# Kernel tuning notes

Measured on AMD Instinct MI355X. Metric: run time of the kernel, lower is better.

Reference implementation:

```python
import jax, jax.numpy as jnp
import numpy as np

# LSNNParameters defaults (norse)
TAU_SYN_INV = 200.0     # 1/tau_syn
TAU_MEM_INV = 100.0     # 1/tau_mem
TAU_ADAPT_INV = 1.0 / 800.0  # 1/tau_adapt
V_LEAK = 0.0
V_TH = 1.0
V_RESET = 0.0
BETA = 1.8
DT = 0.001

B, IN_F, OUT_F = 8192, 512, 1024


def setup_inputs() -> dict:
    key = jax.random.key(0)
    k0, k1, k2, k3, k4, k5, k6 = jax.random.split(key, 7)
    input_spikes = (jax.random.uniform(k0, (B, IN_F)) < 0.2).astype(jnp.float32)
    z = (jax.random.uniform(k1, (B, OUT_F)) < 0.2).astype(jnp.float32)
    v = jax.random.normal(k2, (B, OUT_F)) * 0.5
    i = jax.random.normal(k3, (B, OUT_F)) * 0.5
    b = jax.random.uniform(k4, (B, OUT_F))
    input_weights = jax.random.normal(k5, (OUT_F, IN_F)) / np.sqrt(IN_F)
    recurrent_weights = jax.random.normal(k6, (OUT_F, OUT_F))
    return {
        "input_spikes": input_spikes,
        "z": z,
        "v": v,
        "i": i,
        "b": b,
        "input_weights": input_weights,
        "recurrent_weights": recurrent_weights,
    }


def reference(input_spikes, z, v, i, b, input_weights, recurrent_weights):
    # One euler step of the LSNN cell (norse lsnn_step).
    # voltage update: dv = dt * tau_mem_inv * ((v_leak - v) + i)
    v_decayed = v + DT * TAU_MEM_INV * ((V_LEAK - v) + i)
    # current decay: di = -dt * tau_syn_inv * i
    i_decayed = i + DT * (-TAU_SYN_INV) * i
    # adaptive threshold relaxes toward v_th
    b_decayed = b + DT * TAU_ADAPT_INV * (V_TH - b)
    # spike condition (heaviside jump)
    z_new = (v_decayed - b_decayed > 0).astype(v.dtype)
    # reset
    v_new = (1.0 - z_new) * v_decayed + z_new * V_RESET
    # current jumps from input + recurrent synapses (x @ W^T, torch linear)
    i_new = (
        i_decayed
        + jnp.einsum("bi,oi->bo", input_spikes, input_weights)
        + jnp.einsum("bo,no->bn", z, recurrent_weights)
    )
    # threshold adaptation
    b_new = b_decayed + z_new * TAU_ADAPT_INV * BETA
    # stack (z, v, i, b) new state -> [4, B, OUT_F]
    return jnp.stack([z_new, v_new, i_new, b_new])
```

## Files before the change

### kernel.cpp

```cpp
#include <hip/hip_runtime.h>

#define B_ROWS 8192
#define IN_F 512
#define OUT_F 1024
#define K_TOT 1536

#define BM 128
#define BN 128
#define BK 64
#define LDST 72

typedef short bfrag __attribute__((ext_vector_type(8)));
typedef float f4    __attribute__((ext_vector_type(4)));

__device__ __forceinline__ unsigned int pack2bf(float a, float b) {
    unsigned int ua = __float_as_uint(a);
    unsigned int ub = __float_as_uint(b);
    ua = (ua + 0x7fffu + ((ua >> 16) & 1u)) >> 16;
    ub = (ub + 0x7fffu + ((ub >> 16) & 1u)) & 0xffff0000u;
    return ua | ub;
}

__global__ __launch_bounds__(256, 2) void lsnn_step(
    const float* __restrict__ spikes,
    const float* __restrict__ zin,
    const float* __restrict__ vin,
    const float* __restrict__ iin,
    const float* __restrict__ bin,
    const float* __restrict__ Wi,
    const float* __restrict__ Wr,
    float* __restrict__ out)
{
    __shared__ unsigned short As[BM * LDST];
    __shared__ unsigned short Ws[BN * LDST];

    const int tid = threadIdx.x;
    const int bid = blockIdx.x;
    const int n0 = (bid & 7) * BN;
    const int m0 = (bid >> 3) * BM;

    const int lane = tid & 63;
    const int wave = tid >> 6;
    const int wm = (wave >> 1) * 64;
    const int wn = (wave & 1) * 64;
    const int lr = lane & 15;
    const int lq = lane >> 4;

    const int srow = tid >> 4;
    const int scol = (tid & 15) * 4;

    f4 acc[4][4];
    #pragma unroll
    for (int a = 0; a < 4; ++a)
        #pragma unroll
        for (int b = 0; b < 4; ++b)
            acc[a][b] = (f4)0.0f;

    for (int kt = 0; kt < K_TOT; kt += BK) {
        const float* ap; const float* wp; int ast, wst;
        if (kt < IN_F) {
            ap = spikes + (size_t)m0 * IN_F + kt;            ast = IN_F;
            wp = Wi     + (size_t)n0 * IN_F + kt;            wst = IN_F;
        } else {
            ap = zin + (size_t)m0 * OUT_F + (kt - IN_F);     ast = OUT_F;
            wp = Wr  + (size_t)n0 * OUT_F + (kt - IN_F);     wst = OUT_F;
        }

        float4 fa[8], fw[8];
        #pragma unroll
        for (int p = 0; p < 8; ++p) {
            const int r = srow + p * 16;
            fa[p] = *(const float4*)(ap + (size_t)r * ast + scol);
            fw[p] = *(const float4*)(wp + (size_t)r * wst + scol);
        }
        __syncthreads();
        #pragma unroll
        for (int p = 0; p < 8; ++p) {
            const int r = srow + p * 16;
            *(unsigned int*)&As[r * LDST + scol]     = pack2bf(fa[p].x, fa[p].y);
            *(unsigned int*)&As[r * LDST + scol + 2] = pack2bf(fa[p].z, fa[p].w);
            *(unsigned int*)&Ws[r * LDST + scol]     = pack2bf(fw[p].x, fw[p].y);
            *(unsigned int*)&Ws[r * LDST + scol + 2] = pack2bf(fw[p].z, fw[p].w);
        }
        __syncthreads();

        #pragma unroll
        for (int ks = 0; ks < 2; ++ks) {
            const int kk = ks * 32 + lq * 8;
            bfrag af[4], wf[4];
            #pragma unroll
            for (int t = 0; t < 4; ++t) {
                af[t] = *(const bfrag*)&As[(wm + t * 16 + lr) * LDST + kk];
                wf[t] = *(const bfrag*)&Ws[(wn + t * 16 + lr) * LDST + kk];
            }
            #pragma unroll
            for (int tm = 0; tm < 4; ++tm)
                #pragma unroll
                for (int tn = 0; tn < 4; ++tn)
                    acc[tm][tn] = __builtin_amdgcn_mfma_f32_16x16x32_bf16(
                        af[tm], wf[tn], acc[tm][tn], 0, 0, 0);
        }
    }

    const size_t PL = (size_t)B_ROWS * OUT_F;
    #pragma unroll
    for (int tm = 0; tm < 4; ++tm) {
        #pragma unroll
        for (int tn = 0; tn < 4; ++tn) {
            #pragma unroll
            for (int r = 0; r < 4; ++r) {
                const int gm = m0 + wm + tm * 16 + lq * 4 + r;
                const int gn = n0 + wn + tn * 16 + lr;
                const size_t idx = (size_t)gm * OUT_F + gn;
                const float v = vin[idx];
                const float i = iin[idx];
                const float b = bin[idx];
                const float v_dec = v + 0.1f * ((0.0f - v) + i);
                const float i_dec = i + (-0.2f) * i;
                const float b_dec = b + 1.25e-06f * (1.0f - b);
                const float zn = (v_dec - b_dec > 0.0f) ? 1.0f : 0.0f;
                const float vn = (1.0f - zn) * v_dec;
                const float inew = i_dec + acc[tm][tn][r];
                const float bnew = b_dec + zn * 0.00225f;
                out[idx]          = zn;
                out[PL + idx]     = vn;
                out[2 * PL + idx] = inew;
                out[3 * PL + idx] = bnew;
            }
        }
    }
}

extern "C" void kernel_launch(void* const* d_in, const int* in_sizes, int n_in,
                              void* d_out, int out_size, void* d_ws, size_t ws_size,
                              hipStream_t stream) {
    const float* spikes = (const float*)d_in[0];
    const float* z      = (const float*)d_in[1];
    const float* v      = (const float*)d_in[2];
    const float* i      = (const float*)d_in[3];
    const float* b      = (const float*)d_in[4];
    const float* Wi     = (const float*)d_in[5];
    const float* Wr     = (const float*)d_in[6];
    float* out = (float*)d_out;

    const int grid = (B_ROWS / BM) * (OUT_F / BN);
    lsnn_step<<<grid, 256, 0, stream>>>(spikes, z, v, i, b, Wi, Wr, out);
}
```

Baseline: 347.5 us.

## Halve M tile, prefetch next K tile into registers, raise occupancy

New measurement: 316.9 us. 1.1x faster.

```diff
diff --git a/kernel.cpp b/kernel.cpp
--- a/kernel.cpp
+++ b/kernel.cpp
@@ -5,10 +5,11 @@
 #define OUT_F 1024
 #define K_TOT 1536
 
-#define BM 128
+#define BM 64
 #define BN 128
 #define BK 64
 #define LDST 72
+#define NITER (K_TOT / BK)
 
 typedef short bfrag __attribute__((ext_vector_type(8)));
 typedef float f4    __attribute__((ext_vector_type(4)));
@@ -21,7 +22,7 @@
     return ua | ub;
 }
 
-__global__ __launch_bounds__(256, 2) void lsnn_step(
+__global__ __launch_bounds__(256, 4) void lsnn_step(
     const float* __restrict__ spikes,
     const float* __restrict__ zin,
     const float* __restrict__ vin,
@@ -41,62 +42,71 @@
 
     const int lane = tid & 63;
     const int wave = tid >> 6;
-    const int wm = (wave >> 1) * 64;
-    const int wn = (wave & 1) * 64;
+    const int wn = wave * 32;
     const int lr = lane & 15;
     const int lq = lane >> 4;
 
     const int srow = tid >> 4;
     const int scol = (tid & 15) * 4;
 
-    f4 acc[4][4];
+    f4 acc[4][2];
     #pragma unroll
     for (int a = 0; a < 4; ++a)
         #pragma unroll
-        for (int b = 0; b < 4; ++b)
+        for (int b = 0; b < 2; ++b)
             acc[a][b] = (f4)0.0f;
 
-    for (int kt = 0; kt < K_TOT; kt += BK) {
+    float4 fa[4], fw[8];
+
+    auto load_tile = [&](int kt) {
         const float* ap; const float* wp; int ast, wst;
         if (kt < IN_F) {
-            ap = spikes + (size_t)m0 * IN_F + kt;            ast = IN_F;
-            wp = Wi     + (size_t)n0 * IN_F + kt;            wst = IN_F;
+            ap = spikes + (size_t)m0 * IN_F + kt;          ast = IN_F;
+            wp = Wi     + (size_t)n0 * IN_F + kt;          wst = IN_F;
         } else {
-            ap = zin + (size_t)m0 * OUT_F + (kt - IN_F);     ast = OUT_F;
-            wp = Wr  + (size_t)n0 * OUT_F + (kt - IN_F);     wst = OUT_F;
+            ap = zin + (size_t)m0 * OUT_F + (kt - IN_F);   ast = OUT_F;
+            wp = Wr  + (size_t)n0 * OUT_F + (kt - IN_F);   wst = OUT_F;
         }
+        #pragma unroll
+        for (int p = 0; p < 4; ++p)
+            fa[p] = *(const float4*)(ap + (size_t)(srow + p * 16) * ast + scol);
+        #pragma unroll
+        for (int p = 0; p < 8; ++p)
+            fw[p] = *(const float4*)(wp + (size_t)(srow + p * 16) * wst + scol);
+    };
 
-        float4 fa[8], fw[8];
+    load_tile(0);
+
+    for (int it = 0; it < NITER; ++it) {
+        __syncthreads();
+        #pragma unroll
+        for (int p = 0; p < 4; ++p) {
+            uint2 pk = { pack2bf(fa[p].x, fa[p].y), pack2bf(fa[p].z, fa[p].w) };
+            *(uint2*)&As[(srow + p * 16) * LDST + scol] = pk;
+        }
         #pragma unroll
         for (int p = 0; p < 8; ++p) {
-            const int r = srow + p * 16;
-            fa[p] = *(const float4*)(ap + (size_t)r * ast + scol);
-            fw[p] = *(const float4*)(wp + (size_t)r * wst + scol);
+            uint2 pk = { pack2bf(fw[p].x, fw[p].y), pack2bf(fw[p].z, fw[p].w) };
+            *(uint2*)&Ws[(srow + p * 16) * LDST + scol] = pk;
         }
         __syncthreads();
-        #pragma unroll
-        for (int p = 0; p < 8; ++p) {
-            const int r = srow + p * 16;
-            *(unsigned int*)&As[r * LDST + scol]     = pack2bf(fa[p].x, fa[p].y);
-            *(unsigned int*)&As[r * LDST + scol + 2] = pack2bf(fa[p].z, fa[p].w);
-            *(unsigned int*)&Ws[r * LDST + scol]     = pack2bf(fw[p].x, fw[p].y);
-            *(unsigned int*)&Ws[r * LDST + scol + 2] = pack2bf(fw[p].z, fw[p].w);
-        }
-        __syncthreads();
+
+        if (it + 1 < NITER) load_tile((it + 1) * BK);
 
         #pragma unroll
         for (int ks = 0; ks < 2; ++ks) {
             const int kk = ks * 32 + lq * 8;
-            bfrag af[4], wf[4];
+            bfrag af[4], wf[2];
             #pragma unroll
-            for (int t = 0; t < 4; ++t) {
-                af[t] = *(const bfrag*)&As[(wm + t * 16 + lr) * LDST + kk];
+            for (int t = 0; t < 4; ++t)
+                af[t] = *(const bfrag*)&As[(t * 16 + lr) * LDST + kk];
+            #pragma unroll
+            for (int t = 0; t < 2; ++t)
                 wf[t] = *(const bfrag*)&Ws[(wn + t * 16 + lr) * LDST + kk];
-            }
             #pragma unroll
             for (int tm = 0; tm < 4; ++tm)
                 #pragma unroll
-                for (int tn = 0; tn < 4; ++tn)
+                for (int tn = 0; tn < 2; ++tn)
                     acc[tm][tn] = __builtin_amdgcn_mfma_f32_16x16x32_bf16(
                         af[tm], wf[tn], acc[tm][tn], 0, 0, 0);
         }
@@ -106,17 +116,17 @@
     #pragma unroll
     for (int tm = 0; tm < 4; ++tm) {
         #pragma unroll
-        for (int tn = 0; tn < 4; ++tn) {
+        for (int tn = 0; tn < 2; ++tn) {
             #pragma unroll
             for (int r = 0; r < 4; ++r) {
-                const int gm = m0 + wm + tm * 16 + lq * 4 + r;
+                const int gm = m0 + tm * 16 + lq * 4 + r;
                 const int gn = n0 + wn + tn * 16 + lr;
                 const size_t idx = (size_t)gm * OUT_F + gn;
                 const float v = vin[idx];
                 const float i = iin[idx];
                 const float b = bin[idx];
                 const float v_dec = v + 0.1f * ((0.0f - v) + i);
-                const float i_dec = i + (-0.2f) * i;
+                const float i_dec = i - 0.2f * i;
                 const float b_dec = b + 1.25e-06f * (1.0f - b);
                 const float zn = (v_dec - b_dec > 0.0f) ? 1.0f : 0.0f;
                 const float vn = (1.0f - zn) * v_dec;
```

## Precast GEMM operands to bf16 and stream tiles via global_load_lds

Applied to the files above, without the earlier changes.

New measurement: 340.3 us. 2.1% less time.

```diff
diff --git a/kernel.cpp b/kernel.cpp
--- a/kernel.cpp
+++ b/kernel.cpp
@@ -8,10 +8,16 @@
 #define BM 128
 #define BN 128
 #define BK 64
-#define LDST 72
+#define NITER (K_TOT / BK)
+
+#define A4_COUNT (B_ROWS * (K_TOT / 4))
+#define W4_COUNT (OUT_F  * (K_TOT / 4))
 
 typedef short bfrag __attribute__((ext_vector_type(8)));
 typedef float f4    __attribute__((ext_vector_type(4)));
+
+typedef __attribute__((address_space(3))) unsigned short lds_us;
+typedef __attribute__((address_space(1))) const unsigned short gbl_us;
 
 __device__ __forceinline__ unsigned int pack2bf(float a, float b) {
     unsigned int ua = __float_as_uint(a);
@@ -21,18 +27,41 @@
     return ua | ub;
 }
 
-__global__ __launch_bounds__(256, 2) void lsnn_step(
-    const float* __restrict__ spikes,
-    const float* __restrict__ zin,
+__global__ __launch_bounds__(256) void precast(
+    const float* __restrict__ spikes, const float* __restrict__ zin,
+    const float* __restrict__ Wi,     const float* __restrict__ Wr,
+    unsigned short* __restrict__ Abf, unsigned short* __restrict__ Wbf)
+{
+    const int idx = blockIdx.x * 256 + threadIdx.x;
+    const float* src;
+    unsigned short* dst;
+    if (idx < A4_COUNT) {
+        const int row = idx / 384, c4 = idx - row * 384;
+        src = (c4 < 128) ? spikes + (size_t)row * IN_F + c4 * 4
+                         : zin    + (size_t)row * OUT_F + (c4 - 128) * 4;
+        dst = Abf + (size_t)idx * 4;
+    } else {
+        const int w = idx - A4_COUNT;
+        const int row = w / 384, c4 = w - row * 384;
+        src = (c4 < 128) ? Wi + (size_t)row * IN_F + c4 * 4
+                         : Wr + (size_t)row * OUT_F + (c4 - 128) * 4;
+        dst = Wbf + (size_t)w * 4;
+    }
+    const float4 v = *(const float4*)src;
+    uint2 pk = { pack2bf(v.x, v.y), pack2bf(v.z, v.w) };
+    *(uint2*)dst = pk;
+}
+
+__global__ __launch_bounds__(256, 2) void lsnn_gemm(
+    const unsigned short* __restrict__ Abf,
+    const unsigned short* __restrict__ Wbf,
     const float* __restrict__ vin,
     const float* __restrict__ iin,
     const float* __restrict__ bin,
-    const float* __restrict__ Wi,
-    const float* __restrict__ Wr,
     float* __restrict__ out)
 {
-    __shared__ unsigned short As[BM * LDST];
-    __shared__ unsigned short Ws[BN * LDST];
+    __shared__ unsigned short As[BM * BK];
+    __shared__ unsigned short Ws[BN * BK];
 
     const int tid = threadIdx.x;
     const int bid = blockIdx.x;
@@ -46,9 +75,6 @@
     const int lr = lane & 15;
     const int lq = lane >> 4;
 
-    const int srow = tid >> 4;
-    const int scol = (tid & 15) * 4;
-
     f4 acc[4][4];
     #pragma unroll
     for (int a = 0; a < 4; ++a)
@@ -56,31 +82,32 @@
         for (int b = 0; b < 4; ++b)
             acc[a][b] = (f4)0.0f;
 
-    for (int kt = 0; kt < K_TOT; kt += BK) {
-        const float* ap; const float* wp; int ast, wst;
-        if (kt < IN_F) {
-            ap = spikes + (size_t)m0 * IN_F + kt;            ast = IN_F;
-            wp = Wi     + (size_t)n0 * IN_F + kt;            wst = IN_F;
-        } else {
-            ap = zin + (size_t)m0 * OUT_F + (kt - IN_F);     ast = OUT_F;
-            wp = Wr  + (size_t)n0 * OUT_F + (kt - IN_F);     wst = OUT_F;
+    const unsigned short* Ab = Abf + (size_t)m0 * K_TOT;
+    const unsigned short* Wb = Wbf + (size_t)n0 * K_TOT;
+
+    for (int it = 0; it < NITER; ++it) {
+        const int kt = it * BK;
+        __syncthreads();
+
+        #pragma unroll
+        for (int p = 0; p < 4; ++p) {
+            const int j0 = p * 256 + wave * 64;
+            const int j  = j0 + lane;
+            const int row = j >> 3, c16 = j & 7;
+            __builtin_amdgcn_global_load_lds(
+                (const __attribute__((address_space(1))) void*)(Ab + (size_t)row * K_TOT + kt + c16 * 8),
+                (__attribute__((address_space(3))) void*)(As + j0 * 8),
+                16, 0, 0);
         }
-
-        float4 fa[8], fw[8];
         #pragma unroll
-        for (int p = 0; p < 8; ++p) {
-            const int r = srow + p * 16;
-            fa[p] = *(const float4*)(ap + (size_t)r * ast + scol);
-            fw[p] = *(const float4*)(wp + (size_t)r * wst + scol);
-        }
-        __syncthreads();
-        #pragma unroll
-        for (int p = 0; p < 8; ++p) {
-            const int r = srow + p * 16;
-            *(unsigned int*)&As[r * LDST + scol]     = pack2bf(fa[p].x, fa[p].y);
-            *(unsigned int*)&As[r * LDST + scol + 2] = pack2bf(fa[p].z, fa[p].w);
-            *(unsigned int*)&Ws[r * LDST + scol]     = pack2bf(fw[p].x, fw[p].y);
-            *(unsigned int*)&Ws[r * LDST + scol + 2] = pack2bf(fw[p].z, fw[p].w);
+        for (int p = 0; p < 4; ++p) {
+            const int j0 = p * 256 + wave * 64;
+            const int j  = j0 + lane;
+            const int row = j >> 3, c16 = j & 7;
+            __builtin_amdgcn_global_load_lds(
+                (const __attribute__((address_space(1))) void*)(Wb + (size_t)row * K_TOT + kt + c16 * 8),
+                (__attribute__((address_space(3))) void*)(Ws + j0 * 8),
+                16, 0, 0);
         }
         __syncthreads();
 
@@ -90,8 +117,8 @@
             bfrag af[4], wf[4];
             #pragma unroll
             for (int t = 0; t < 4; ++t) {
-                af[t] = *(const bfrag*)&As[(wm + t * 16 + lr) * LDST + kk];
-                wf[t] = *(const bfrag*)&Ws[(wn + t * 16 + lr) * LDST + kk];
+                af[t] = *(const bfrag*)&As[(wm + t * 16 + lr) * BK + kk];
+                wf[t] = *(const bfrag*)&Ws[(wn + t * 16 + lr) * BK + kk];
             }
             #pragma unroll
             for (int tm = 0; tm < 4; ++tm)
@@ -116,7 +143,7 @@
                 const float i = iin[idx];
                 const float b = bin[idx];
                 const float v_dec = v + 0.1f * ((0.0f - v) + i);
-                const float i_dec = i + (-0.2f) * i;
+                const float i_dec = i - 0.2f * i;
                 const float b_dec = b + 1.25e-06f * (1.0f - b);
                 const float zn = (v_dec - b_dec > 0.0f) ? 1.0f : 0.0f;
                 const float vn = (1.0f - zn) * v_dec;
@@ -143,6 +170,12 @@
     const float* Wr     = (const float*)d_in[6];
     float* out = (float*)d_out;
 
+    unsigned short* Abf = (unsigned short*)d_ws;
+    unsigned short* Wbf = Abf + (size_t)B_ROWS * K_TOT;
+
+    const int pc_grid = (A4_COUNT + W4_COUNT) / 256;
+    precast<<<pc_grid, 256, 0, stream>>>(spikes, z, Wi, Wr, Abf, Wbf);
+
     const int grid = (B_ROWS / BM) * (OUT_F / BN);
-    lsnn_step<<<grid, 256, 0, stream>>>(spikes, z, v, i, b, Wi, Wr, out);
+    lsnn_gemm<<<grid, 256, 0, stream>>>(Abf, Wbf, v, i, b, out);
 }
```
